# Optimization experiments

Hardware: AMD Instinct MI355X
Metric: run time of the kernel (lower is better)

Reference implementation:

```python
import jax, jax.numpy as jnp
import numpy as np

NUM_HEADS = 4


def _mha_pool(seg):
    """seg: [n_seg, S, H]. First 4 channels are attention logits (softmax over S),
    rest are values split into 4 heads; returns [n_seg, H-4]."""
    n_seg, S, H = seg.shape
    attn = jax.nn.softmax(seg[:, :, :NUM_HEADS], axis=1)          # [n, S, 4]
    vals = seg[:, :, NUM_HEADS:].reshape(n_seg, S, NUM_HEADS, -1)  # [n, S, 4, hd]
    pooled = jnp.einsum('nsh,nshd->nhd', attn, vals)               # [n, 4, hd]
    return pooled.reshape(n_seg, -1)


def setup_inputs() -> dict:
    key = jax.random.key(0)
    k1, k2, k3, k4 = jax.random.split(key, 4)
    T, D, H = 131072, 2048, 260
    embeddings = jax.random.normal(k1, (T, D), dtype=jnp.float32)
    labels = jax.random.randint(k2, (T,), 0, 2, dtype=jnp.int32)
    W_down = jax.random.normal(k3, (D, H), dtype=jnp.float32) / np.sqrt(D)
    b_down = jnp.zeros((H,), dtype=jnp.float32)
    W_final = jax.random.normal(k4, (H - NUM_HEADS, 1), dtype=jnp.float32) / np.sqrt(H - NUM_HEADS)
    b_final = jnp.zeros((1,), dtype=jnp.float32)
    return {
        'embeddings': embeddings,
        'W_down': W_down,
        'b_down': b_down,
        'W_final': W_final,
        'b_final': b_final,
        'labels': labels,
        'tokens_per_problem': 512,
        'tokens_per_line': 16,
    }


def reference(embeddings, W_down, b_down, W_final, b_final, labels,
              tokens_per_problem, tokens_per_line):
    T, D = embeddings.shape
    H = W_down.shape[1]
    # Dropout is identity in eval mode (reference baseline).
    proj = embeddings @ W_down + b_down                      # [T, H]
    # MHA_POOL_4_HEADS: keep attention logits raw, GELU (exact erf) the values.
    act = jnp.concatenate(
        [proj[:, :NUM_HEADS], jax.nn.gelu(proj[:, NUM_HEADS:], approximate=False)],
        axis=1)                                              # [T, H]

    P = T // tokens_per_problem
    problem_feat = _mha_pool(act.reshape(P, tokens_per_problem, H))   # [P, H-4]
    problem_logits = (problem_feat @ W_final + b_final)[:, 0]

    L = T // tokens_per_line
    line_feat = _mha_pool(act.reshape(L, tokens_per_line, H))         # [L, H-4]
    line_logits = (line_feat @ W_final + b_final)[:, 0]

    token_logits = (act[:, NUM_HEADS:] @ W_final + b_final)[:, 0]     # [T]

    problem_labels = labels.reshape(P, tokens_per_problem).min(axis=1)
    line_labels = labels.reshape(L, tokens_per_line).min(axis=1)
    return token_logits, line_logits, line_labels, problem_logits, problem_labels
```

## Files before the change

### kernel.cpp

```cpp
#include <hip/hip_runtime.h>
#include <hip/hip_bf16.h>
#include <math.h>

#define T_TOK   131072
#define D_IN    2048
#define H_CH    260
#define NFRAG   17
#define KSTEPS  64
#define STEP_BYTES  (NFRAG * 64 * 16)
#define CHUNK_BYTES (2 * STEP_BYTES)
#define NCHUNK  32

typedef __attribute__((ext_vector_type(8))) short bf16x8;
typedef __attribute__((ext_vector_type(4))) float f32x4;

__device__ inline short f2bf(float x) {
    __hip_bfloat16 h = __float2bfloat16(x);
    return __builtin_bit_cast(short, h);
}

__global__ void prep_wfrag(const float* __restrict__ W, __hip_bfloat16* __restrict__ Wf) {
    int g = blockIdx.x;
    int s = g / NFRAG, f = g % NFRAG;
    int lane = threadIdx.x;
    int k0 = s * 32 + (lane >> 4) * 8;
    int col = f * 16 + (lane & 15);
    short vals8[8];
#pragma unroll
    for (int j = 0; j < 8; j++) {
        float v = (col < H_CH) ? W[(size_t)(k0 + j) * H_CH + col] : 0.f;
        vals8[j] = f2bf(v);
    }
    *reinterpret_cast<bf16x8*>(reinterpret_cast<short*>(Wf) + ((size_t)g * 64 + lane) * 8) =
        *reinterpret_cast<bf16x8*>(vals8);
}

__global__ __launch_bounds__(256, 2)
void gemm_act(const float* __restrict__ emb, const __hip_bfloat16* __restrict__ Wfrag,
              const float* __restrict__ b_down, const float* __restrict__ W_final,
              const float* __restrict__ b_final,
              float* __restrict__ attnL, __hip_bfloat16* __restrict__ vals,
              float* __restrict__ token_logits) {
    __shared__ __align__(16) char smem[2 * CHUNK_BYTES];

    int wave = threadIdx.x >> 6;
    int lane = threadIdx.x & 63;
    int r0 = blockIdx.x * 128 + wave * 32;
    int row_in = lane & 15;
    int kbase = (lane >> 4) * 8;

    const char* gW = (const char*)Wfrag;

    auto stage_chunk = [&](int c, char* lbase) {
        const char* src = gW + (size_t)c * CHUNK_BYTES;
#pragma unroll
        for (int r = 0; r < 8; ++r) {
            int off = (r * 256 + wave * 64) * 16;
            __builtin_amdgcn_global_load_lds(
                (const __attribute__((address_space(1))) unsigned int*)(src + off + lane * 16),
                (__attribute__((address_space(3))) unsigned int*)(lbase + off), 16, 0, 0);
        }
        if (wave < 2) {
            int off = (8 * 256 + wave * 64) * 16;
            __builtin_amdgcn_global_load_lds(
                (const __attribute__((address_space(1))) unsigned int*)(src + off + lane * 16),
                (__attribute__((address_space(3))) unsigned int*)(lbase + off), 16, 0, 0);
        }
    };

    f32x4 acc0[NFRAG], acc1[NFRAG];
#pragma unroll
    for (int f = 0; f < NFRAG; f++) {
        acc0[f] = (f32x4){0.f, 0.f, 0.f, 0.f};
        acc1[f] = (f32x4){0.f, 0.f, 0.f, 0.f};
    }

    const float* ap0 = emb + (size_t)(r0 + row_in) * D_IN + kbase;
    const float* ap1 = ap0 + (size_t)16 * D_IN;

    stage_chunk(0, smem);
    f32x4 c0l = *reinterpret_cast<const f32x4*>(ap0);
    f32x4 c0h = *reinterpret_cast<const f32x4*>(ap0 + 4);
    f32x4 c1l = *reinterpret_cast<const f32x4*>(ap1);
    f32x4 c1h = *reinterpret_cast<const f32x4*>(ap1 + 4);
    f32x4 n0l, n0h, n1l, n1h;
    __syncthreads();

#define DO_STEP(AL0, AH0, AL1, AH1, BOFF)                                         \
    {                                                                             \
        bf16x8 af0, af1;                                                          \
        af0[0] = f2bf(AL0[0]); af0[1] = f2bf(AL0[1]);                             \
        af0[2] = f2bf(AL0[2]); af0[3] = f2bf(AL0[3]);                             \
        af0[4] = f2bf(AH0[0]); af0[5] = f2bf(AH0[1]);                             \
        af0[6] = f2bf(AH0[2]); af0[7] = f2bf(AH0[3]);                             \
        af1[0] = f2bf(AL1[0]); af1[1] = f2bf(AL1[1]);                             \
        af1[2] = f2bf(AL1[2]); af1[3] = f2bf(AL1[3]);                             \
        af1[4] = f2bf(AH1[0]); af1[5] = f2bf(AH1[1]);                             \
        af1[6] = f2bf(AH1[2]); af1[7] = f2bf(AH1[3]);                             \
        const char* bb = smem + (BOFF) + lane * 16;                               \
        _Pragma("unroll")                                                         \
        for (int f = 0; f < NFRAG; f++) {                                         \
            bf16x8 bfr = *reinterpret_cast<const bf16x8*>(bb + f * 1024);         \
            acc0[f] = __builtin_amdgcn_mfma_f32_16x16x32_bf16(af0, bfr, acc0[f], 0, 0, 0); \
            acc1[f] = __builtin_amdgcn_mfma_f32_16x16x32_bf16(af1, bfr, acc1[f], 0, 0, 0); \
        }                                                                         \
    }

    for (int c = 0; c < NCHUNK; ++c) {
        int base = (c & 1) * CHUNK_BYTES;
        if (c + 1 < NCHUNK) stage_chunk(c + 1, smem + ((c + 1) & 1) * CHUNK_BYTES);

        int s1 = 2 * c + 1;
        int off1 = s1 * 32;
        n0l = *reinterpret_cast<const f32x4*>(ap0 + off1);
        n0h = *reinterpret_cast<const f32x4*>(ap0 + off1 + 4);
        n1l = *reinterpret_cast<const f32x4*>(ap1 + off1);
        n1h = *reinterpret_cast<const f32x4*>(ap1 + off1 + 4);
        DO_STEP(c0l, c0h, c1l, c1h, base);

        int s2 = 2 * c + 2;
        int off2 = (s2 < KSTEPS ? s2 : 0) * 32;
        c0l = *reinterpret_cast<const f32x4*>(ap0 + off2);
        c0h = *reinterpret_cast<const f32x4*>(ap0 + off2 + 4);
        c1l = *reinterpret_cast<const f32x4*>(ap1 + off2);
        c1h = *reinterpret_cast<const f32x4*>(ap1 + off2 + 4);
        DO_STEP(n0l, n0h, n1l, n1h, base + STEP_BYTES);

        __syncthreads();
    }
#undef DO_STEP

    int colbase = lane & 15;
    int rgroup = (lane >> 4) * 4;
    float tp0[4] = {0.f, 0.f, 0.f, 0.f};
    float tp1[4] = {0.f, 0.f, 0.f, 0.f};
#pragma unroll
    for (int f = 0; f < NFRAG; f++) {
        int n = f * 16 + colbase;
        float bias = (n < H_CH) ? b_down[n] : 0.f;
        float wf = (n >= 4 && n < H_CH) ? W_final[n - 4] : 0.f;
#pragma unroll
        for (int i = 0; i < 4; i++) {
            int row0 = r0 + rgroup + i;
            int row1 = row0 + 16;
            float v0 = acc0[f][i] + bias;
            float v1 = acc1[f][i] + bias;
            float a0 = (n < 4) ? v0 : 0.5f * v0 * (1.f + erff(v0 * 0.70710678118f));
            float a1 = (n < 4) ? v1 : 0.5f * v1 * (1.f + erff(v1 * 0.70710678118f));
            if (n < 4) {
                attnL[(size_t)row0 * 4 + n] = v0;
                attnL[(size_t)row1 * 4 + n] = v1;
            } else if (n < H_CH) {
                vals[(size_t)row0 * 256 + (n - 4)] = __float2bfloat16(a0);
                vals[(size_t)row1 * 256 + (n - 4)] = __float2bfloat16(a1);
            }
            tp0[i] += a0 * wf;
            tp1[i] += a1 * wf;
        }
    }
#pragma unroll
    for (int i = 0; i < 4; i++) {
        float v0 = tp0[i], v1 = tp1[i];
        v0 += __shfl_xor(v0, 1); v1 += __shfl_xor(v1, 1);
        v0 += __shfl_xor(v0, 2); v1 += __shfl_xor(v1, 2);
        v0 += __shfl_xor(v0, 4); v1 += __shfl_xor(v1, 4);
        v0 += __shfl_xor(v0, 8); v1 += __shfl_xor(v1, 8);
        if ((lane & 15) == 0) {
            token_logits[r0 + rgroup + i]      = v0 + b_final[0];
            token_logits[r0 + 16 + rgroup + i] = v1 + b_final[0];
        }
    }
}

__global__ __launch_bounds__(256)
void pool_problem(const float* __restrict__ attnL, const __hip_bfloat16* __restrict__ vals,
                  const int* __restrict__ labels,
                  const float* __restrict__ W_final, const float* __restrict__ b_final,
                  float* __restrict__ out_logits, float* __restrict__ out_labels) {
    __shared__ float w_lds[512 * 4];
    __shared__ float wred[4][4];
    __shared__ float psum[4];
    __shared__ int   lred[4];

    int p = blockIdx.x;
    int t = threadIdx.x;
    int lane = t & 63, wid = t >> 6;
    const float* abase = attnL + (size_t)p * 512 * 4;

    f32x4 v0 = *reinterpret_cast<const f32x4*>(abase + (size_t)t * 4);
    f32x4 v1 = *reinterpret_cast<const f32x4*>(abase + (size_t)(t + 256) * 4);

    float mh[4];
#pragma unroll
    for (int h = 0; h < 4; h++) mh[h] = fmaxf(v0[h], v1[h]);
#pragma unroll
    for (int h = 0; h < 4; h++)
        for (int mask = 1; mask < 64; mask <<= 1) mh[h] = fmaxf(mh[h], __shfl_xor(mh[h], mask));
    if (lane == 0) {
#pragma unroll
        for (int h = 0; h < 4; h++) wred[wid][h] = mh[h];
    }
    __syncthreads();
#pragma unroll
    for (int h = 0; h < 4; h++)
        mh[h] = fmaxf(fmaxf(wred[0][h], wred[1][h]), fmaxf(wred[2][h], wred[3][h]));
    __syncthreads();

    float Zh[4];
    f32x4 e0, e1;
#pragma unroll
    for (int h = 0; h < 4; h++) {
        e0[h] = __expf(v0[h] - mh[h]);
        e1[h] = __expf(v1[h] - mh[h]);
        Zh[h] = e0[h] + e1[h];
    }
    *reinterpret_cast<f32x4*>(&w_lds[t * 4]) = e0;
    *reinterpret_cast<f32x4*>(&w_lds[(t + 256) * 4]) = e1;
#pragma unroll
    for (int h = 0; h < 4; h++)
        for (int mask = 1; mask < 64; mask <<= 1) Zh[h] += __shfl_xor(Zh[h], mask);
    if (lane == 0) {
#pragma unroll
        for (int h = 0; h < 4; h++) wred[wid][h] = Zh[h];
    }
    __syncthreads();
#pragma unroll
    for (int h = 0; h < 4; h++) Zh[h] = wred[0][h] + wred[1][h] + wred[2][h] + wred[3][h];

    int h = t >> 6;
    const __hip_bfloat16* col = vals + (size_t)p * 512 * 256 + t;
    float pooled = 0.f;
#pragma unroll 8
    for (int s = 0; s < 512; s++)
        pooled += w_lds[s * 4 + h] * __bfloat162float(col[(size_t)s * 256]);
    float part = (pooled / Zh[h]) * W_final[t];
    for (int mask = 1; mask < 64; mask <<= 1) part += __shfl_xor(part, mask);
    if (lane == 0) psum[wid] = part;

    int lmin = min(labels[p * 512 + t], labels[p * 512 + t + 256]);
    for (int mask = 1; mask < 64; mask <<= 1) lmin = min(lmin, __shfl_xor(lmin, mask));
    if (lane == 0) lred[wid] = lmin;
    __syncthreads();
    if (t == 0) {
        out_logits[p] = psum[0] + psum[1] + psum[2] + psum[3] + b_final[0];
        out_labels[p] = (float)min(min(lred[0], lred[1]), min(lred[2], lred[3]));
    }
}

__global__ __launch_bounds__(256)
void pool_line(const float* __restrict__ attnL, const __hip_bfloat16* __restrict__ vals,
               const int* __restrict__ labels,
               const float* __restrict__ W_final, const float* __restrict__ b_final,
               float* __restrict__ out_logits, float* __restrict__ out_labels) {
    int wid = threadIdx.x >> 6, lane = threadIdx.x & 63;
    int line = blockIdx.x * 4 + wid;

    float x = attnL[(size_t)line * 64 + lane];
    float mm = x;
    mm = fmaxf(mm, __shfl_xor(mm, 4));
    mm = fmaxf(mm, __shfl_xor(mm, 8));
    mm = fmaxf(mm, __shfl_xor(mm, 16));
    mm = fmaxf(mm, __shfl_xor(mm, 32));
    float e = __expf(x - mm);
    float Z = e;
    Z += __shfl_xor(Z, 4);
    Z += __shfl_xor(Z, 8);
    Z += __shfl_xor(Z, 16);
    Z += __shfl_xor(Z, 32);
    float w = e / Z;

    const __hip_bfloat16* vbase = vals + (size_t)line * 16 * 256;
    float logit_part = 0.f;
#pragma unroll
    for (int j = 0; j < 4; j++) {
        float pooled = 0.f;
#pragma unroll
        for (int s = 0; s < 16; s++) {
            float ws = __shfl(w, s * 4 + j);
            pooled += ws * __bfloat162float(vbase[(size_t)s * 256 + j * 64 + lane]);
        }
        logit_part += pooled * W_final[j * 64 + lane];
    }
    for (int mask = 1; mask < 64; mask <<= 1) logit_part += __shfl_xor(logit_part, mask);

    int lab = (lane < 16) ? labels[line * 16 + lane] : 0x7fffffff;
    for (int mask = 1; mask < 64; mask <<= 1) lab = min(lab, __shfl_xor(lab, mask));

    if (lane == 0) {
        out_logits[line] = logit_part + b_final[0];
        out_labels[line] = (float)lab;
    }
}

extern "C" void kernel_launch(void* const* d_in, const int* in_sizes, int n_in,
                              void* d_out, int out_size, void* d_ws, size_t ws_size,
                              hipStream_t stream) {
    const float* emb     = (const float*)d_in[0];
    const float* W_down  = (const float*)d_in[1];
    const float* b_down  = (const float*)d_in[2];
    const float* W_final = (const float*)d_in[3];
    const float* b_final = (const float*)d_in[4];
    const int*   labels  = (const int*)d_in[5];

    float* out      = (float*)d_out;
    float* tok      = out;
    float* line_lg  = out + 131072;
    float* line_lb  = out + 139264;
    float* prob_lg  = out + 147456;
    float* prob_lb  = out + 147712;

    __hip_bfloat16* Wfrag = (__hip_bfloat16*)d_ws;
    float* attnL = (float*)((char*)d_ws + ((size_t)4 << 20));
    __hip_bfloat16* vals = (__hip_bfloat16*)((char*)d_ws + ((size_t)8 << 20));

    prep_wfrag<<<KSTEPS * NFRAG, 64, 0, stream>>>(W_down, Wfrag);
    gemm_act<<<T_TOK / 128, 256, 0, stream>>>(emb, Wfrag, b_down, W_final, b_final,
                                              attnL, vals, tok);
    pool_problem<<<256, 256, 0, stream>>>(attnL, vals, labels, W_final, b_final, prob_lg, prob_lb);
    pool_line<<<2048, 256, 0, stream>>>(attnL, vals, labels, W_final, b_final, line_lg, line_lb);
}
```

Baseline: 408.3 us.

## Split GEMM work across 8 waves of 16 rows each to raise occupancy

The gemm_act block grows from 4 to 8 waves, and each wave now owns 16 rows instead of 32. That halves the accumulator registers per wave and raises the launch-bounds target to 4 blocks of 512 threads. The weight staging is redistributed across 8 waves. The aim is more waves in flight to hide the global A loads and LDS latency. The cost is that each B fragment read from LDS now feeds only one MFMA instead of two, doubling LDS read traffic per FLOP, while LDS use per block (about 70 KB) may cap how many blocks fit.

```diff
diff --git a/kernel.cpp b/kernel.cpp
--- a/kernel.cpp
+++ b/kernel.cpp
@@ -35,7 +35,7 @@
         *reinterpret_cast<bf16x8*>(vals8);
 }
 
-__global__ __launch_bounds__(256, 2)
+__global__ __launch_bounds__(512, 4)
 void gemm_act(const float* __restrict__ emb, const __hip_bfloat16* __restrict__ Wfrag,
               const float* __restrict__ b_down, const float* __restrict__ W_final,
               const float* __restrict__ b_final,
@@ -45,7 +45,7 @@
 
     int wave = threadIdx.x >> 6;
     int lane = threadIdx.x & 63;
-    int r0 = blockIdx.x * 128 + wave * 32;
+    int r0 = blockIdx.x * 128 + wave * 16;
     int row_in = lane & 15;
     int kbase = (lane >> 4) * 8;
 
@@ -54,55 +54,44 @@
     auto stage_chunk = [&](int c, char* lbase) {
         const char* src = gW + (size_t)c * CHUNK_BYTES;
 #pragma unroll
-        for (int r = 0; r < 8; ++r) {
-            int off = (r * 256 + wave * 64) * 16;
+        for (int r = 0; r < 4; ++r) {
+            int off = (r * 8 + wave) * 1024;
             __builtin_amdgcn_global_load_lds(
                 (const __attribute__((address_space(1))) unsigned int*)(src + off + lane * 16),
                 (__attribute__((address_space(3))) unsigned int*)(lbase + off), 16, 0, 0);
         }
         if (wave < 2) {
-            int off = (8 * 256 + wave * 64) * 16;
+            int off = (32 + wave) * 1024;
             __builtin_amdgcn_global_load_lds(
                 (const __attribute__((address_space(1))) unsigned int*)(src + off + lane * 16),
                 (__attribute__((address_space(3))) unsigned int*)(lbase + off), 16, 0, 0);
         }
     };
 
-    f32x4 acc0[NFRAG], acc1[NFRAG];
-#pragma unroll
-    for (int f = 0; f < NFRAG; f++) {
-        acc0[f] = (f32x4){0.f, 0.f, 0.f, 0.f};
-        acc1[f] = (f32x4){0.f, 0.f, 0.f, 0.f};
-    }
-
-    const float* ap0 = emb + (size_t)(r0 + row_in) * D_IN + kbase;
-    const float* ap1 = ap0 + (size_t)16 * D_IN;
+    f32x4 acc[NFRAG];
+#pragma unroll
+    for (int f = 0; f < NFRAG; f++) acc[f] = (f32x4){0.f, 0.f, 0.f, 0.f};
+
+    const float* aptr = emb + (size_t)(r0 + row_in) * D_IN + kbase;
 
     stage_chunk(0, smem);
-    f32x4 c0l = *reinterpret_cast<const f32x4*>(ap0);
-    f32x4 c0h = *reinterpret_cast<const f32x4*>(ap0 + 4);
-    f32x4 c1l = *reinterpret_cast<const f32x4*>(ap1);
-    f32x4 c1h = *reinterpret_cast<const f32x4*>(ap1 + 4);
-    f32x4 n0l, n0h, n1l, n1h;
-    __syncthreads();
-
-#define DO_STEP(AL0, AH0, AL1, AH1, BOFF)                                         \
+    f32x4 cl = *reinterpret_cast<const f32x4*>(aptr);
+    f32x4 ch = *reinterpret_cast<const f32x4*>(aptr + 4);
+    f32x4 nl, nh;
+    __syncthreads();
+
+#define DO_STEP(AL, AH, BOFF)                                                     \
     {                                                                             \
-        bf16x8 af0, af1;                                                          \
-        af0[0] = f2bf(AL0[0]); af0[1] = f2bf(AL0[1]);                             \
-        af0[2] = f2bf(AL0[2]); af0[3] = f2bf(AL0[3]);                             \
-        af0[4] = f2bf(AH0[0]); af0[5] = f2bf(AH0[1]);                             \
-        af0[6] = f2bf(AH0[2]); af0[7] = f2bf(AH0[3]);                             \
-        af1[0] = f2bf(AL1[0]); af1[1] = f2bf(AL1[1]);                             \
-        af1[2] = f2bf(AL1[2]); af1[3] = f2bf(AL1[3]);                             \
-        af1[4] = f2bf(AH1[0]); af1[5] = f2bf(AH1[1]);                             \
-        af1[6] = f2bf(AH1[2]); af1[7] = f2bf(AH1[3]);                             \
+        bf16x8 af;                                                                \
+        af[0] = f2bf(AL[0]); af[1] = f2bf(AL[1]);                                 \
+        af[2] = f2bf(AL[2]); af[3] = f2bf(AL[3]);                                 \
+        af[4] = f2bf(AH[0]); af[5] = f2bf(AH[1]);                                 \
+        af[6] = f2bf(AH[2]); af[7] = f2bf(AH[3]);                                 \
         const char* bb = smem + (BOFF) + lane * 16;                               \
         _Pragma("unroll")                                                         \
         for (int f = 0; f < NFRAG; f++) {                                         \
             bf16x8 bfr = *reinterpret_cast<const bf16x8*>(bb + f * 1024);         \
-            acc0[f] = __builtin_amdgcn_mfma_f32_16x16x32_bf16(af0, bfr, acc0[f], 0, 0, 0); \
-            acc1[f] = __builtin_amdgcn_mfma_f32_16x16x32_bf16(af1, bfr, acc1[f], 0, 0, 0); \
+            acc[f] = __builtin_amdgcn_mfma_f32_16x16x32_bf16(af, bfr, acc[f], 0, 0, 0); \
         }                                                                         \
     }
 
@@ -110,21 +99,16 @@
         int base = (c & 1) * CHUNK_BYTES;
         if (c + 1 < NCHUNK) stage_chunk(c + 1, smem + ((c + 1) & 1) * CHUNK_BYTES);
 
-        int s1 = 2 * c + 1;
-        int off1 = s1 * 32;
-        n0l = *reinterpret_cast<const f32x4*>(ap0 + off1);
-        n0h = *reinterpret_cast<const f32x4*>(ap0 + off1 + 4);
-        n1l = *reinterpret_cast<const f32x4*>(ap1 + off1);
-        n1h = *reinterpret_cast<const f32x4*>(ap1 + off1 + 4);
-        DO_STEP(c0l, c0h, c1l, c1h, base);
+        int off1 = (2 * c + 1) * 32;
+        nl = *reinterpret_cast<const f32x4*>(aptr + off1);
+        nh = *reinterpret_cast<const f32x4*>(aptr + off1 + 4);
+        DO_STEP(cl, ch, base)
 
         int s2 = 2 * c + 2;
         int off2 = (s2 < KSTEPS ? s2 : 0) * 32;
-        c0l = *reinterpret_cast<const f32x4*>(ap0 + off2);
-        c0h = *reinterpret_cast<const f32x4*>(ap0 + off2 + 4);
-        c1l = *reinterpret_cast<const f32x4*>(ap1 + off2);
-        c1h = *reinterpret_cast<const f32x4*>(ap1 + off2 + 4);
-        DO_STEP(n0l, n0h, n1l, n1h, base + STEP_BYTES);
+        cl = *reinterpret_cast<const f32x4*>(aptr + off2);
+        ch = *reinterpret_cast<const f32x4*>(aptr + off2 + 4);
+        DO_STEP(nl, nh, base + STEP_BYTES)
 
         __syncthreads();
     }
@@ -132,8 +116,7 @@
 
     int colbase = lane & 15;
     int rgroup = (lane >> 4) * 4;
-    float tp0[4] = {0.f, 0.f, 0.f, 0.f};
-    float tp1[4] = {0.f, 0.f, 0.f, 0.f};
+    float tp[4] = {0.f, 0.f, 0.f, 0.f};
 #pragma unroll
     for (int f = 0; f < NFRAG; f++) {
         int n = f * 16 + colbase;
@@ -141,34 +124,25 @@
         float wf = (n >= 4 && n < H_CH) ? W_final[n - 4] : 0.f;
 #pragma unroll
         for (int i = 0; i < 4; i++) {
-            int row0 = r0 + rgroup + i;
-            int row1 = row0 + 16;
-            float v0 = acc0[f][i] + bias;
-            float v1 = acc1[f][i] + bias;
-            float a0 = (n < 4) ? v0 : 0.5f * v0 * (1.f + erff(v0 * 0.70710678118f));
-            float a1 = (n < 4) ? v1 : 0.5f * v1 * (1.f + erff(v1 * 0.70710678118f));
+            int row = r0 + rgroup + i;
+            float v = acc[f][i] + bias;
+            float a = (n < 4) ? v : 0.5f * v * (1.f + erff(v * 0.70710678118f));
             if (n < 4) {
-                attnL[(size_t)row0 * 4 + n] = v0;
-                attnL[(size_t)row1 * 4 + n] = v1;
+                attnL[(size_t)row * 4 + n] = v;
             } else if (n < H_CH) {
-                vals[(size_t)row0 * 256 + (n - 4)] = __float2bfloat16(a0);
-                vals[(size_t)row1 * 256 + (n - 4)] = __float2bfloat16(a1);
+                vals[(size_t)row * 256 + (n - 4)] = __float2bfloat16(a);
             }
-            tp0[i] += a0 * wf;
-            tp1[i] += a1 * wf;
+            tp[i] += a * wf;
         }
     }
 #pragma unroll
     for (int i = 0; i < 4; i++) {
-        float v0 = tp0[i], v1 = tp1[i];
-        v0 += __shfl_xor(v0, 1); v1 += __shfl_xor(v1, 1);
-        v0 += __shfl_xor(v0, 2); v1 += __shfl_xor(v1, 2);
-        v0 += __shfl_xor(v0, 4); v1 += __shfl_xor(v1, 4);
-        v0 += __shfl_xor(v0, 8); v1 += __shfl_xor(v1, 8);
-        if ((lane & 15) == 0) {
-            token_logits[r0 + rgroup + i]      = v0 + b_final[0];
-            token_logits[r0 + 16 + rgroup + i] = v1 + b_final[0];
-        }
+        float v = tp[i];
+        v += __shfl_xor(v, 1);
+        v += __shfl_xor(v, 2);
+        v += __shfl_xor(v, 4);
+        v += __shfl_xor(v, 8);
+        if ((lane & 15) == 0) token_logits[r0 + rgroup + i] = v + b_final[0];
     }
 }
 
@@ -314,7 +288,7 @@
     __hip_bfloat16* vals = (__hip_bfloat16*)((char*)d_ws + ((size_t)8 << 20));
 
     prep_wfrag<<<KSTEPS * NFRAG, 64, 0, stream>>>(W_down, Wfrag);
-    gemm_act<<<T_TOK / 128, 256, 0, stream>>>(emb, Wfrag, b_down, W_final, b_final,
+    gemm_act<<<T_TOK / 128, 512, 0, stream>>>(emb, Wfrag, b_down, W_final, b_final,
                                               attnL, vals, tok);
     pool_problem<<<256, 256, 0, stream>>>(attnL, vals, labels, W_final, b_final, prob_lg, prob_lb);
     pool_line<<<2048, 256, 0, stream>>>(attnL, vals, labels, W_final, b_final, line_lg, line_lb);
```

After: 352.8 us. 1.16x faster.

## Split GEMM output columns across two wave groups with 512-thread blocks

Applied to the files above, without the earlier changes.

Doubles the gemm_act block to 512 threads. The second group of four waves covers the upper 8 of the 17 N-fragments for the same 128 rows, which roughly halves the accumulator registers per wave so more waves can be resident. The B-tile staging is spread over 8 waves, and the token-logit partial sums from the two halves are combined through a small shared-memory reduction. The cost is that every A row is loaded and converted to bf16 twice, once per wave half. The two halves are also imbalanced (9 vs 8 fragments), and an extra barrier is added at the end.

```diff
diff --git a/kernel.cpp b/kernel.cpp
--- a/kernel.cpp
+++ b/kernel.cpp
@@ -35,17 +35,22 @@
         *reinterpret_cast<bf16x8*>(vals8);
 }
 
-__global__ __launch_bounds__(256, 2)
+__global__ __launch_bounds__(512, 4)
 void gemm_act(const float* __restrict__ emb, const __hip_bfloat16* __restrict__ Wfrag,
               const float* __restrict__ b_down, const float* __restrict__ W_final,
               const float* __restrict__ b_final,
               float* __restrict__ attnL, __hip_bfloat16* __restrict__ vals,
               float* __restrict__ token_logits) {
     __shared__ __align__(16) char smem[2 * CHUNK_BYTES];
+    __shared__ float tokred[8][32];
 
     int wave = threadIdx.x >> 6;
     int lane = threadIdx.x & 63;
-    int r0 = blockIdx.x * 128 + wave * 32;
+    int quad = wave & 3;
+    int nhalf = wave >> 2;
+    int f0 = nhalf ? 9 : 0;
+    int nf = nhalf ? 8 : 9;
+    int r0 = blockIdx.x * 128 + quad * 32;
     int row_in = lane & 15;
     int kbase = (lane >> 4) * 8;
 
@@ -54,23 +59,23 @@
     auto stage_chunk = [&](int c, char* lbase) {
         const char* src = gW + (size_t)c * CHUNK_BYTES;
 #pragma unroll
-        for (int r = 0; r < 8; ++r) {
-            int off = (r * 256 + wave * 64) * 16;
+        for (int r = 0; r < 4; ++r) {
+            int off = (r * 8 + wave) * 1024;
             __builtin_amdgcn_global_load_lds(
                 (const __attribute__((address_space(1))) unsigned int*)(src + off + lane * 16),
                 (__attribute__((address_space(3))) unsigned int*)(lbase + off), 16, 0, 0);
         }
         if (wave < 2) {
-            int off = (8 * 256 + wave * 64) * 16;
+            int off = (32 + wave) * 1024;
             __builtin_amdgcn_global_load_lds(
                 (const __attribute__((address_space(1))) unsigned int*)(src + off + lane * 16),
                 (__attribute__((address_space(3))) unsigned int*)(lbase + off), 16, 0, 0);
         }
     };
 
-    f32x4 acc0[NFRAG], acc1[NFRAG];
-#pragma unroll
-    for (int f = 0; f < NFRAG; f++) {
+    f32x4 acc0[9], acc1[9];
+#pragma unroll
+    for (int f = 0; f < 9; f++) {
         acc0[f] = (f32x4){0.f, 0.f, 0.f, 0.f};
         acc1[f] = (f32x4){0.f, 0.f, 0.f, 0.f};
     }
@@ -97,12 +102,14 @@
         af1[2] = f2bf(AL1[2]); af1[3] = f2bf(AL1[3]);                             \
         af1[4] = f2bf(AH1[0]); af1[5] = f2bf(AH1[1]);                             \
         af1[6] = f2bf(AH1[2]); af1[7] = f2bf(AH1[3]);                             \
-        const char* bb = smem + (BOFF) + lane * 16;                               \
+        const char* bb = smem + (BOFF) + (size_t)f0 * 1024 + lane * 16;           \
         _Pragma("unroll")                                                         \
-        for (int f = 0; f < NFRAG; f++) {                                         \
-            bf16x8 bfr = *reinterpret_cast<const bf16x8*>(bb + f * 1024);         \
-            acc0[f] = __builtin_amdgcn_mfma_f32_16x16x32_bf16(af0, bfr, acc0[f], 0, 0, 0); \
-            acc1[f] = __builtin_amdgcn_mfma_f32_16x16x32_bf16(af1, bfr, acc1[f], 0, 0, 0); \
+        for (int f = 0; f < 9; f++) {                                             \
+            if (f < nf) {                                                         \
+                bf16x8 bfr = *reinterpret_cast<const bf16x8*>(bb + f * 1024);     \
+                acc0[f] = __builtin_amdgcn_mfma_f32_16x16x32_bf16(af0, bfr, acc0[f], 0, 0, 0); \
+                acc1[f] = __builtin_amdgcn_mfma_f32_16x16x32_bf16(af1, bfr, acc1[f], 0, 0, 0); \
+            }                                                                     \
         }                                                                         \
     }
 
@@ -110,13 +117,12 @@
         int base = (c & 1) * CHUNK_BYTES;
         if (c + 1 < NCHUNK) stage_chunk(c + 1, smem + ((c + 1) & 1) * CHUNK_BYTES);
 
-        int s1 = 2 * c + 1;
-        int off1 = s1 * 32;
+        int off1 = (2 * c + 1) * 32;
         n0l = *reinterpret_cast<const f32x4*>(ap0 + off1);
         n0h = *reinterpret_cast<const f32x4*>(ap0 + off1 + 4);
         n1l = *reinterpret_cast<const f32x4*>(ap1 + off1);
         n1h = *reinterpret_cast<const f32x4*>(ap1 + off1 + 4);
-        DO_STEP(c0l, c0h, c1l, c1h, base);
+        DO_STEP(c0l, c0h, c1l, c1h, base)
 
         int s2 = 2 * c + 2;
         int off2 = (s2 < KSTEPS ? s2 : 0) * 32;
@@ -124,7 +130,7 @@
         c0h = *reinterpret_cast<const f32x4*>(ap0 + off2 + 4);
         c1l = *reinterpret_cast<const f32x4*>(ap1 + off2);
         c1h = *reinterpret_cast<const f32x4*>(ap1 + off2 + 4);
-        DO_STEP(n0l, n0h, n1l, n1h, base + STEP_BYTES);
+        DO_STEP(n0l, n0h, n1l, n1h, base + STEP_BYTES)
 
         __syncthreads();
     }
@@ -135,27 +141,29 @@
     float tp0[4] = {0.f, 0.f, 0.f, 0.f};
     float tp1[4] = {0.f, 0.f, 0.f, 0.f};
 #pragma unroll
-    for (int f = 0; f < NFRAG; f++) {
-        int n = f * 16 + colbase;
-        float bias = (n < H_CH) ? b_down[n] : 0.f;
-        float wf = (n >= 4 && n < H_CH) ? W_final[n - 4] : 0.f;
-#pragma unroll
-        for (int i = 0; i < 4; i++) {
-            int row0 = r0 + rgroup + i;
-            int row1 = row0 + 16;
-            float v0 = acc0[f][i] + bias;
-            float v1 = acc1[f][i] + bias;
-            float a0 = (n < 4) ? v0 : 0.5f * v0 * (1.f + erff(v0 * 0.70710678118f));
-            float a1 = (n < 4) ? v1 : 0.5f * v1 * (1.f + erff(v1 * 0.70710678118f));
-            if (n < 4) {
-                attnL[(size_t)row0 * 4 + n] = v0;
-                attnL[(size_t)row1 * 4 + n] = v1;
-            } else if (n < H_CH) {
-                vals[(size_t)row0 * 256 + (n - 4)] = __float2bfloat16(a0);
-                vals[(size_t)row1 * 256 + (n - 4)] = __float2bfloat16(a1);
+    for (int f = 0; f < 9; f++) {
+        if (f < nf) {
+            int n = (f0 + f) * 16 + colbase;
+            float bias = (n < H_CH) ? b_down[n] : 0.f;
+            float wf = (n >= 4 && n < H_CH) ? W_final[n - 4] : 0.f;
+#pragma unroll
+            for (int i = 0; i < 4; i++) {
+                int row0 = r0 + rgroup + i;
+                int row1 = row0 + 16;
+                float v0 = acc0[f][i] + bias;
+                float v1 = acc1[f][i] + bias;
+                float a0 = (n < 4) ? v0 : 0.5f * v0 * (1.f + erff(v0 * 0.70710678118f));
+                float a1 = (n < 4) ? v1 : 0.5f * v1 * (1.f + erff(v1 * 0.70710678118f));
+                if (n < 4) {
+                    attnL[(size_t)row0 * 4 + n] = v0;
+                    attnL[(size_t)row1 * 4 + n] = v1;
+                } else if (n < H_CH) {
+                    vals[(size_t)row0 * 256 + (n - 4)] = __float2bfloat16(a0);
+                    vals[(size_t)row1 * 256 + (n - 4)] = __float2bfloat16(a1);
+                }
+                tp0[i] += a0 * wf;
+                tp1[i] += a1 * wf;
             }
-            tp0[i] += a0 * wf;
-            tp1[i] += a1 * wf;
         }
     }
 #pragma unroll
@@ -166,9 +174,15 @@
         v0 += __shfl_xor(v0, 4); v1 += __shfl_xor(v1, 4);
         v0 += __shfl_xor(v0, 8); v1 += __shfl_xor(v1, 8);
         if ((lane & 15) == 0) {
-            token_logits[r0 + rgroup + i]      = v0 + b_final[0];
-            token_logits[r0 + 16 + rgroup + i] = v1 + b_final[0];
-        }
+            tokred[wave][rgroup + i]      = v0;
+            tokred[wave][16 + rgroup + i] = v1;
+        }
+    }
+    __syncthreads();
+    if (threadIdx.x < 128) {
+        int q = threadIdx.x >> 5, j = threadIdx.x & 31;
+        token_logits[blockIdx.x * 128 + q * 32 + j] =
+            tokred[q][j] + tokred[4 + q][j] + b_final[0];
     }
 }
 
@@ -314,7 +328,7 @@
     __hip_bfloat16* vals = (__hip_bfloat16*)((char*)d_ws + ((size_t)8 << 20));
 
     prep_wfrag<<<KSTEPS * NFRAG, 64, 0, stream>>>(W_down, Wfrag);
-    gemm_act<<<T_TOK / 128, 256, 0, stream>>>(emb, Wfrag, b_down, W_final, b_final,
+    gemm_act<<<T_TOK / 128, 512, 0, stream>>>(emb, Wfrag, b_down, W_final, b_final,
                                               attnL, vals, tok);
     pool_problem<<<256, 256, 0, stream>>>(attnL, vals, labels, W_final, b_final, prob_lg, prob_lb);
     pool_line<<<2048, 256, 0, stream>>>(attnL, vals, labels, W_final, b_final, line_lg, line_lb);
```

Result: slower. 456.2 us (+11.7%).
